# Kernel tuning notes

Hardware: AMD Instinct MI355X
Metric: run time of the kernel (lower is better)

The kernel has to match this reference:

```python
import jax, jax.numpy as jnp
import numpy as np

D_MODEL = 512
NUM_HEADS = 8
NUM_LAYERS = 4
SEQ_LEN = 2048
BATCH = 2
LN_EPS = 1e-5


def _layer_norm(x, g, b):
    mu = jnp.mean(x, axis=-1, keepdims=True)
    var = jnp.mean(jnp.square(x - mu), axis=-1, keepdims=True)
    return (x - mu) * jax.lax.rsqrt(var + LN_EPS) * g + b


def setup_inputs() -> dict:
    key = jax.random.key(0)
    ks = jax.random.split(key, 12)
    d, nl = D_MODEL, NUM_LAYERS
    s = 0.02
    return {
        "x": jax.random.normal(ks[0], (BATCH, SEQ_LEN, d), dtype=jnp.float32),
        "mask": jnp.zeros((1, 1, SEQ_LEN, SEQ_LEN), dtype=jnp.float32),
        "Wqkv": jax.random.normal(ks[1], (nl, d, 3 * d), dtype=jnp.float32) * s,
        "Wout": jax.random.normal(ks[2], (nl, d, d), dtype=jnp.float32) * s,
        "ln_g": jnp.ones((nl, d), dtype=jnp.float32),
        "ln_b": jnp.zeros((nl, d), dtype=jnp.float32),
        "W1": jax.random.normal(ks[3], (nl, d, 4 * d), dtype=jnp.float32) * s,
        "b1": jnp.zeros((nl, 4 * d), dtype=jnp.float32),
        "alpha": jnp.full((nl,), 0.01, dtype=jnp.float32),  # PReLU(init=0.01), scalar per block
        "W2": jax.random.normal(ks[4], (nl, 4 * d, d), dtype=jnp.float32) * s,
        "b2": jnp.zeros((nl, d), dtype=jnp.float32),
        "lnf_g": jnp.ones((d,), dtype=jnp.float32),
        "lnf_b": jnp.zeros((d,), dtype=jnp.float32),
    }


def _encoder(x, mask, Wqkv, Wout, ln_g, ln_b, W1, b1, alpha, W2, b2, lnf_g, lnf_b):
    B, L, d = x.shape
    H = NUM_HEADS
    dh = d // H
    scale = 1.0 / (d ** 0.5)  # NOTE: scales by sqrt(d_model), not head dim (as in source)

    def block(x, p):
        wqkv, wout, g, b, w1, b1_, a, w2, b2_ = p
        qkv = x @ wqkv  # [B, L, 3d]
        q, k, v = jnp.split(qkv, 3, axis=-1)
        # b l (h j) -> b h l j
        to_heads = lambda t: t.reshape(B, L, H, dh).transpose(0, 2, 1, 3)
        q, k, v = to_heads(q) * scale, to_heads(k), to_heads(v)
        e = jnp.einsum('bhlj,bhkj->bhlk', q, k) + mask  # [B, H, L, L]
        att = jnp.nan_to_num(jax.nn.softmax(e, axis=-1))
        # Faithful to source: repeated index takes the DIAGONAL of att,
        # then multiplies elementwise into v (NOT a matmul).
        out = jnp.einsum('bhll,bhlj->bhlj', att, v)
        out = out.transpose(0, 2, 1, 3).reshape(B, L, d)  # b h l j -> b l (h j)
        out = out @ wout
        out_att = _layer_norm(out + x, g, b)
        h = out_att @ w1 + b1_
        h = jnp.where(h >= 0, h, a * h)  # PReLU (dropout=0 in eval)
        h = h @ w2 + b2_
        # same LayerNorm params reused (same nn.LayerNorm instance in source)
        return _layer_norm(h + out_att, g, b), None

    params = (Wqkv, Wout, ln_g, ln_b, W1, b1, alpha, W2, b2)
    x, _ = jax.lax.scan(block, x, params)
    return _layer_norm(x, lnf_g, lnf_b)


def reference(x, mask, Wqkv, Wout, ln_g, ln_b, W1, b1, alpha, W2, b2, lnf_g, lnf_b):
    return _encoder(x, mask, Wqkv, Wout, ln_g, ln_b, W1, b1, alpha, W2, b2, lnf_g, lnf_b)
```

## Files before the change

### kernel.cpp

```cpp
#include <hip/hip_runtime.h>
#include <math.h>

typedef unsigned short u16;
typedef __attribute__((ext_vector_type(8))) short short8;
typedef __attribute__((ext_vector_type(4))) float f32x4;

#define SEQ 2048
#define NHEADS 8
#define NLAYERS 4
#define NROWS 4096
#define SCALE_QK_LOG2E 0.06376571201f
#define PART_STRIDE ((size_t)NROWS * 512)

#define GLOAD_LDS(gp, lp) __builtin_amdgcn_global_load_lds( \
    (const __attribute__((address_space(1))) uint4*)(gp), \
    (__attribute__((address_space(3))) uint4*)(lp), 16, 0, 0)

__device__ __forceinline__ float b2f(u16 u){
    union { unsigned int i; float f; } c; c.i = ((unsigned int)u) << 16; return c.f;
}
__device__ __forceinline__ u16 f2b(float f){
    union { float f; unsigned int i; } c; c.f = f;
    unsigned int x = c.i;
    unsigned int r = x + 0x7fffu + ((x >> 16) & 1u);
    return (u16)(r >> 16);
}
__device__ __forceinline__ void unpack8(uint4 u, float* f){
    f[0]=b2f(u.x & 0xffffu); f[1]=b2f(u.x >> 16);
    f[2]=b2f(u.y & 0xffffu); f[3]=b2f(u.y >> 16);
    f[4]=b2f(u.z & 0xffffu); f[5]=b2f(u.z >> 16);
    f[6]=b2f(u.w & 0xffffu); f[7]=b2f(u.w >> 16);
}
__device__ __forceinline__ uint4 pack8(const float* f){
    uint4 u;
    u.x = (unsigned)f2b(f[0]) | ((unsigned)f2b(f[1]) << 16);
    u.y = (unsigned)f2b(f[2]) | ((unsigned)f2b(f[3]) << 16);
    u.z = (unsigned)f2b(f[4]) | ((unsigned)f2b(f[5]) << 16);
    u.w = (unsigned)f2b(f[6]) | ((unsigned)f2b(f[7]) << 16);
    return u;
}

__global__ __launch_bounds__(256)
void cvt_f32_bf16(const float* __restrict__ in, u16* __restrict__ out, int n8){
    int i = blockIdx.x * 256 + threadIdx.x;
    if (i >= n8) return;
    const float4* p = (const float4*)(in + (size_t)i * 8);
    float4 a = p[0], b = p[1];
    float f[8] = {a.x, a.y, a.z, a.w, b.x, b.y, b.z, b.w};
    *((uint4*)(out + (size_t)i * 8)) = pack8(f);
}

__global__ __launch_bounds__(256)
void transpose_layer(const float* __restrict__ wqkv, const float* __restrict__ wout,
                     const float* __restrict__ w1,  const float* __restrict__ w2,
                     u16* __restrict__ qkvT, u16* __restrict__ woutT,
                     u16* __restrict__ w1T,  u16* __restrict__ w2T)
{
    __shared__ float tile[32][33];
    int tid = blockIdx.x;
    const float* src; u16* dst; int R, C, local;
    if (tid < 768)       { src = wqkv; dst = qkvT; R = 512;  C = 1536; local = tid; }
    else if (tid < 1024) { src = wout; dst = woutT; R = 512; C = 512;  local = tid - 768; }
    else if (tid < 2048) { src = w1;   dst = w1T;  R = 512;  C = 2048; local = tid - 1024; }
    else                 { src = w2;   dst = w2T;  R = 2048; C = 512;  local = tid - 2048; }
    int ctiles = C >> 5;
    int c0 = (local % ctiles) * 32, r0 = (local / ctiles) * 32;
    int tx = threadIdx.x & 31, ty = threadIdx.x >> 5;
#pragma unroll
    for (int i = 0; i < 4; i++){
        int r = r0 + ty + i * 8;
        tile[ty + i * 8][tx] = src[(size_t)r * C + c0 + tx];
    }
    __syncthreads();
#pragma unroll
    for (int i = 0; i < 4; i++){
        int c = c0 + ty + i * 8;
        dst[(size_t)c * R + r0 + tx] = f2b(tile[tx][ty + i * 8]);
    }
}

template<int BM, int BN, int SPLITS>
__global__ __launch_bounds__(256)
void gemm3(const u16* __restrict__ A, const u16* __restrict__ Bt,
           u16* __restrict__ C,
           const float* __restrict__ bias, const float* __restrict__ alphap,
           int N, int K)
{
    constexpr int NBY = NROWS / BM;
    constexpr int WAVES_M = BM / 64;
    constexpr int WAVES_N = 4 / WAVES_M;
    constexpr int WN = BN / WAVES_N;
    constexpr int MT = 4, NT = WN / 16;
    __shared__ __align__(16) u16 As[BM * 64];
    __shared__ __align__(16) u16 Bs[BN * 64];

    const int t = threadIdx.x;
    const int wave = t >> 6, lane = t & 63;
    const int quad = lane >> 4, l16 = lane & 15;
    const int wm = (WAVES_M == 2) ? (wave >> 1) : 0;
    const int wn = (WAVES_M == 2) ? (wave & 1) : wave;
    const int id = blockIdx.x;
    const int m0 = (id % NBY) * BM;
    const int n0 = (id / NBY) * BN;
    const int lr = lane >> 3;
    const int lc = (lane & 7) << 3;
    const int Ks = K / SPLITS;
    const int kbeg = blockIdx.z * Ks;

    f32x4 acc[MT][NT];
#pragma unroll
    for (int i = 0; i < MT; i++)
#pragma unroll
        for (int j = 0; j < NT; j++) acc[i][j] = (f32x4){0.f, 0.f, 0.f, 0.f};

    for (int kt = kbeg; kt < kbeg + Ks; kt += 64){
        __syncthreads();
#pragma unroll
        for (int j = 0; j < BM / 32; j++){
            int r0 = wave * 8 + j * 32;
            GLOAD_LDS(A + (size_t)(m0 + r0 + lr) * K + kt + lc, As + r0 * 64);
        }
#pragma unroll
        for (int j = 0; j < BN / 32; j++){
            int r0 = wave * 8 + j * 32;
            GLOAD_LDS(Bt + (size_t)(n0 + r0 + lr) * K + kt + lc, Bs + r0 * 64);
        }
        __syncthreads();
#pragma unroll
        for (int ks = 0; ks < 2; ks++){
            short8 af[MT], bf[NT];
#pragma unroll
            for (int mt = 0; mt < MT; mt++)
                af[mt] = *((const short8*)&As[(wm * 64 + mt * 16 + l16) * 64 + ks * 32 + quad * 8]);
#pragma unroll
            for (int nt = 0; nt < NT; nt++)
                bf[nt] = *((const short8*)&Bs[(wn * WN + nt * 16 + l16) * 64 + ks * 32 + quad * 8]);
#pragma unroll
            for (int mt = 0; mt < MT; mt++)
#pragma unroll
                for (int nt = 0; nt < NT; nt++)
                    acc[mt][nt] = __builtin_amdgcn_mfma_f32_16x16x32_bf16(af[mt], bf[nt], acc[mt][nt], 0, 0, 0);
        }
    }

    u16* Cp = (SPLITS > 1) ? (C + (size_t)blockIdx.z * PART_STRIDE) : C;
    const float aval = alphap ? alphap[0] : 0.f;
#pragma unroll
    for (int nt = 0; nt < NT; nt++){
        int col = n0 + wn * WN + nt * 16 + l16;
        float bv = (SPLITS == 1 && bias) ? bias[col] : 0.f;
#pragma unroll
        for (int mt = 0; mt < MT; mt++){
#pragma unroll
            for (int r = 0; r < 4; r++){
                int row = m0 + wm * 64 + mt * 16 + quad * 4 + r;
                float v = acc[mt][nt][r] + bv;
                if (SPLITS == 1 && alphap) v = (v >= 0.f) ? v : aval * v;
                Cp[(size_t)row * N + col] = f2b(v);
            }
        }
    }
}

__global__ __launch_bounds__(256)
void attn_scores2(const u16* __restrict__ qkv, float* __restrict__ rowsum_parts)
{
    __shared__ __align__(16) u16 Qs[128 * 64];
    __shared__ __align__(16) u16 Ks[128 * 64];
    const int t = threadIdx.x, wave = t >> 6, lane = t & 63;
    const int quad = lane >> 4, l16 = lane & 15;
    const int wm = wave >> 1, wn = wave & 1;
    const int id = blockIdx.x;
    const int bh = id & 15, ly = (id >> 4) & 15, ksp = id >> 8;
    const int b = bh >> 3, h = bh & 7;
    const int lr = lane >> 3, lc = (lane & 7) << 3;
    const size_t qbase = (size_t)(b * SEQ + ly * 128) * 1536 + h * 64;

#pragma unroll
    for (int j = 0; j < 4; j++){
        int r0 = wave * 8 + j * 32;
        GLOAD_LDS(qkv + qbase + (size_t)(r0 + lr) * 1536 + lc, Qs + r0 * 64);
    }

    float rs[4][4];
#pragma unroll
    for (int i = 0; i < 4; i++)
#pragma unroll
        for (int j = 0; j < 4; j++) rs[i][j] = 0.f;

    for (int kxi = 0; kxi < 4; kxi++){
        const int kx = ksp * 4 + kxi;
        const size_t kbase = (size_t)(b * SEQ + kx * 128) * 1536 + 512 + h * 64;
        __syncthreads();
#pragma unroll
        for (int j = 0; j < 4; j++){
            int r0 = wave * 8 + j * 32;
            GLOAD_LDS(qkv + kbase + (size_t)(r0 + lr) * 1536 + lc, Ks + r0 * 64);
        }
        __syncthreads();

        f32x4 acc[4][4];
#pragma unroll
        for (int i = 0; i < 4; i++)
#pragma unroll
            for (int j = 0; j < 4; j++) acc[i][j] = (f32x4){0.f, 0.f, 0.f, 0.f};
#pragma unroll
        for (int ks = 0; ks < 2; ks++){
            short8 af[4], bf[4];
#pragma unroll
            for (int mt = 0; mt < 4; mt++)
                af[mt] = *((const short8*)&Qs[(wm * 64 + mt * 16 + l16) * 64 + ks * 32 + quad * 8]);
#pragma unroll
            for (int nt = 0; nt < 4; nt++)
                bf[nt] = *((const short8*)&Ks[(wn * 64 + nt * 16 + l16) * 64 + ks * 32 + quad * 8]);
#pragma unroll
            for (int mt = 0; mt < 4; mt++)
#pragma unroll
                for (int nt = 0; nt < 4; nt++)
                    acc[mt][nt] = __builtin_amdgcn_mfma_f32_16x16x32_bf16(af[mt], bf[nt], acc[mt][nt], 0, 0, 0);
        }
#pragma unroll
        for (int mt = 0; mt < 4; mt++)
#pragma unroll
            for (int nt = 0; nt < 4; nt++)
#pragma unroll
                for (int r = 0; r < 4; r++)
                    rs[mt][r] += exp2f(acc[mt][nt][r] * SCALE_QK_LOG2E);
    }

#pragma unroll
    for (int off = 1; off < 16; off <<= 1){
#pragma unroll
        for (int mt = 0; mt < 4; mt++)
#pragma unroll
            for (int r = 0; r < 4; r++)
                rs[mt][r] += __shfl_xor(rs[mt][r], off, 64);
    }
    if (l16 == 0){
        const int part = ksp * 2 + wn;
        float* dst = rowsum_parts + (size_t)part * 16 * SEQ + (size_t)bh * SEQ + ly * 128;
#pragma unroll
        for (int mt = 0; mt < 4; mt++)
#pragma unroll
            for (int r = 0; r < 4; r++)
                dst[wm * 64 + mt * 16 + quad * 4 + r] = rs[mt][r];
    }
}

__global__ __launch_bounds__(256)
void attn_scale(const u16* __restrict__ qkv, const float* __restrict__ rowsum_parts,
                u16* __restrict__ attnb)
{
    int gid = blockIdx.x * 256 + threadIdx.x;
    int row = gid >> 6;
    int col = (gid & 63) << 3;
    int head = col >> 6;
    int b = row >> 11, l = row & 2047;
    size_t base = (size_t)row * 1536 + col;

    float qv[8], kv[8];
    unpack8(*((const uint4*)(qkv + base)), qv);
    unpack8(*((const uint4*)(qkv + base + 512)), kv);
    float dot = 0.f;
#pragma unroll
    for (int j = 0; j < 8; j++) dot += qv[j] * kv[j];
#pragma unroll
    for (int off = 1; off < 8; off <<= 1) dot += __shfl_xor(dot, off, 64);

    size_t idx = (size_t)(b * 8 + head) * SEQ + l;
    float rsum = 0.f;
#pragma unroll
    for (int p = 0; p < 8; p++) rsum += rowsum_parts[(size_t)p * 16 * SEQ + idx];
    float a = exp2f(dot * SCALE_QK_LOG2E) / rsum;

    float f[8];
    unpack8(*((const uint4*)(qkv + base + 1024)), f);
#pragma unroll
    for (int j = 0; j < 8; j++) f[j] *= a;
    *((uint4*)(attnb + (size_t)row * 512 + col)) = pack8(f);
}

__global__ __launch_bounds__(256)
void ln_kernel(const u16* __restrict__ res, int nparts,
               const float* __restrict__ bias, const u16* __restrict__ xin,
               const float* __restrict__ gg, const float* __restrict__ bb,
               u16* __restrict__ outb, float* __restrict__ outf)
{
    const int row = blockIdx.x * 4 + (threadIdx.x >> 6);
    const int lane = threadIdx.x & 63;
    const size_t base = (size_t)row * 512 + lane * 8;

    float v[8];
    unpack8(*((const uint4*)(xin + base)), v);
    for (int p = 0; p < nparts; p++){
        float rv[8];
        unpack8(*((const uint4*)(res + (size_t)p * PART_STRIDE + base)), rv);
#pragma unroll
        for (int j = 0; j < 8; j++) v[j] += rv[j];
    }
    if (bias){
        const float4* bp4 = (const float4*)(bias + lane * 8);
        float4 c0 = bp4[0], c1 = bp4[1];
        v[0] += c0.x; v[1] += c0.y; v[2] += c0.z; v[3] += c0.w;
        v[4] += c1.x; v[5] += c1.y; v[6] += c1.z; v[7] += c1.w;
    }
    float s = 0.f;
#pragma unroll
    for (int j = 0; j < 8; j++) s += v[j];
#pragma unroll
    for (int off = 32; off; off >>= 1) s += __shfl_xor(s, off, 64);
    float mu = s * (1.f / 512.f);
    float q = 0.f;
#pragma unroll
    for (int j = 0; j < 8; j++){ float d = v[j] - mu; q += d * d; }
#pragma unroll
    for (int off = 32; off; off >>= 1) q += __shfl_xor(q, off, 64);
    float rs = rsqrtf(q * (1.f / 512.f) + 1e-5f);

    const float4* gp = (const float4*)(gg + lane * 8);
    const float4* bp = (const float4*)(bb + lane * 8);
    float4 g0 = gp[0], g1 = gp[1], bb0 = bp[0], bb1 = bp[1];
    float gv[8] = {g0.x, g0.y, g0.z, g0.w, g1.x, g1.y, g1.z, g1.w};
    float bv[8] = {bb0.x, bb0.y, bb0.z, bb0.w, bb1.x, bb1.y, bb1.z, bb1.w};
    float o[8];
#pragma unroll
    for (int j = 0; j < 8; j++) o[j] = (v[j] - mu) * rs * gv[j] + bv[j];
    if (outb){
        *((uint4*)(outb + base)) = pack8(o);
    } else {
        float4* op = (float4*)(outf + base);
        op[0] = make_float4(o[0], o[1], o[2], o[3]);
        op[1] = make_float4(o[4], o[5], o[6], o[7]);
    }
}

extern "C" void kernel_launch(void* const* d_in, const int* in_sizes, int n_in,
                              void* d_out, int out_size, void* d_ws, size_t ws_size,
                              hipStream_t stream)
{
    const float* x_in  = (const float*)d_in[0];
    const float* Wqkv  = (const float*)d_in[2];
    const float* Wout  = (const float*)d_in[3];
    const float* ln_g  = (const float*)d_in[4];
    const float* ln_b  = (const float*)d_in[5];
    const float* W1    = (const float*)d_in[6];
    const float* b1    = (const float*)d_in[7];
    const float* alpha = (const float*)d_in[8];
    const float* W2    = (const float*)d_in[9];
    const float* b2    = (const float*)d_in[10];
    const float* lnf_g = (const float*)d_in[11];
    const float* lnf_b = (const float*)d_in[12];
    float* out = (float*)d_out;

    char* w = (char*)d_ws;
    u16* qkvT  = (u16*)w;  w += (size_t)1536 * 512 * 2;
    u16* woutT = (u16*)w;  w += (size_t)512 * 512 * 2;
    u16* w1T   = (u16*)w;  w += (size_t)2048 * 512 * 2;
    u16* w2T   = (u16*)w;  w += (size_t)512 * 2048 * 2;
    u16* big    = (u16*)w;  w += (size_t)NROWS * 2048 * 2;
    u16* x_cur  = (u16*)w;  w += (size_t)NROWS * 512 * 2;
    u16* attnb  = (u16*)w;  w += (size_t)NROWS * 512 * 2;
    u16* outatt = (u16*)w;  w += (size_t)NROWS * 512 * 2;
    u16* tmpb   = (u16*)w;  w += (size_t)4 * PART_STRIDE * 2;
    float* rowsum_parts = (float*)w; w += (size_t)8 * 2 * NHEADS * SEQ * 4;

    u16* qkvb = big;
    u16* hbuf = big;

    cvt_f32_bf16<<<NROWS * 512 / 8 / 256, 256, 0, stream>>>(x_in, x_cur, NROWS * 512 / 8);

    for (int l = 0; l < NLAYERS; l++){
        transpose_layer<<<3072, 256, 0, stream>>>(
            Wqkv + (size_t)l * 512 * 1536, Wout + (size_t)l * 512 * 512,
            W1 + (size_t)l * 512 * 2048,  W2 + (size_t)l * 2048 * 512,
            qkvT, woutT, w1T, w2T);

        gemm3<128, 64, 1><<<dim3(24 * 32), 256, 0, stream>>>(
            x_cur, qkvT, qkvb, nullptr, nullptr, 1536, 512);

        attn_scores2<<<1024, 256, 0, stream>>>(qkvb, rowsum_parts);
        attn_scale<<<NROWS * 512 / 8 / 256, 256, 0, stream>>>(qkvb, rowsum_parts, attnb);

        gemm3<64, 128, 2><<<dim3(4 * 64, 1, 2), 256, 0, stream>>>(
            attnb, woutT, tmpb, nullptr, nullptr, 512, 512);

        ln_kernel<<<NROWS / 4, 256, 0, stream>>>(tmpb, 2, nullptr, x_cur,
            ln_g + l * 512, ln_b + l * 512, outatt, nullptr);

        gemm3<128, 128, 1><<<dim3(16 * 32), 256, 0, stream>>>(
            outatt, w1T, hbuf, b1 + (size_t)l * 2048, alpha + l, 2048, 512);

        gemm3<64, 128, 4><<<dim3(4 * 64, 1, 4), 256, 0, stream>>>(
            hbuf, w2T, tmpb, nullptr, nullptr, 512, 2048);

        ln_kernel<<<NROWS / 4, 256, 0, stream>>>(tmpb, 4, b2 + (size_t)l * 512, outatt,
            ln_g + l * 512, ln_b + l * 512, x_cur, nullptr);
    }

    ln_kernel<<<NROWS / 4, 256, 0, stream>>>(nullptr, 0, nullptr, x_cur, lnf_g, lnf_b, nullptr, out);
}
```

Baseline: 537.5 us.

## Fuse attention row-sum and diagonal scaling; transpose all layer weights once

The two attention kernels (partial row sums written to global memory, then a separate scale pass) become one 512-thread kernel per (batch, head, 128-row block). It loops over all 16 key tiles, reduces row sums through shared memory, then scales V by the diagonal softmax weight in the same kernel. The per-layer weight transposes are replaced by a single launch covering all layers into a larger workspace. This cuts launches and global traffic, but attention now runs only 256 blocks with serialized key tiles instead of 1024 blocks, which lowers parallelism.

Result: slower. 574.4 us (+6.9%).

```diff
diff --git a/kernel.cpp b/kernel.cpp
--- a/kernel.cpp
+++ b/kernel.cpp
@@ -51,18 +51,19 @@
 }
 
 __global__ __launch_bounds__(256)
-void transpose_layer(const float* __restrict__ wqkv, const float* __restrict__ wout,
-                     const float* __restrict__ w1,  const float* __restrict__ w2,
-                     u16* __restrict__ qkvT, u16* __restrict__ woutT,
-                     u16* __restrict__ w1T,  u16* __restrict__ w2T)
+void transpose_all(const float* __restrict__ Wqkv, const float* __restrict__ Wout,
+                   const float* __restrict__ W1,  const float* __restrict__ W2,
+                   u16* __restrict__ qkvT, u16* __restrict__ woutT,
+                   u16* __restrict__ w1T,  u16* __restrict__ w2T)
 {
     __shared__ float tile[32][33];
-    int tid = blockIdx.x;
+    int l = blockIdx.x / 3072;
+    int tid = blockIdx.x % 3072;
     const float* src; u16* dst; int R, C, local;
-    if (tid < 768)       { src = wqkv; dst = qkvT; R = 512;  C = 1536; local = tid; }
-    else if (tid < 1024) { src = wout; dst = woutT; R = 512; C = 512;  local = tid - 768; }
-    else if (tid < 2048) { src = w1;   dst = w1T;  R = 512;  C = 2048; local = tid - 1024; }
-    else                 { src = w2;   dst = w2T;  R = 2048; C = 512;  local = tid - 2048; }
+    if (tid < 768)       { src = Wqkv + (size_t)l * 512 * 1536; dst = qkvT + (size_t)l * 1536 * 512; R = 512;  C = 1536; local = tid; }
+    else if (tid < 1024) { src = Wout + (size_t)l * 512 * 512;  dst = woutT + (size_t)l * 512 * 512; R = 512;  C = 512;  local = tid - 768; }
+    else if (tid < 2048) { src = W1 + (size_t)l * 512 * 2048;   dst = w1T + (size_t)l * 2048 * 512;  R = 512;  C = 2048; local = tid - 1024; }
+    else                 { src = W2 + (size_t)l * 2048 * 512;   dst = w2T + (size_t)l * 512 * 2048;  R = 2048; C = 512;  local = tid - 2048; }
     int ctiles = C >> 5;
     int c0 = (local % ctiles) * 32, r0 = (local / ctiles) * 32;
     int tx = threadIdx.x & 31, ty = threadIdx.x >> 5;
@@ -162,23 +163,26 @@
     }
 }
 
-__global__ __launch_bounds__(256)
-void attn_scores2(const u16* __restrict__ qkv, float* __restrict__ rowsum_parts)
+__global__ __launch_bounds__(512)
+void attn_fused(const u16* __restrict__ qkv, u16* __restrict__ attnb)
 {
     __shared__ __align__(16) u16 Qs[128 * 64];
     __shared__ __align__(16) u16 Ks[128 * 64];
+    __shared__ float psum[4][128];
+    __shared__ float rowsum[128];
+
     const int t = threadIdx.x, wave = t >> 6, lane = t & 63;
     const int quad = lane >> 4, l16 = lane & 15;
-    const int wm = wave >> 1, wn = wave & 1;
+    const int wm = wave >> 2, wn = wave & 3;
     const int id = blockIdx.x;
-    const int bh = id & 15, ly = (id >> 4) & 15, ksp = id >> 8;
+    const int ly = id & 15, bh = id >> 4;
     const int b = bh >> 3, h = bh & 7;
     const int lr = lane >> 3, lc = (lane & 7) << 3;
     const size_t qbase = (size_t)(b * SEQ + ly * 128) * 1536 + h * 64;
 
 #pragma unroll
-    for (int j = 0; j < 4; j++){
-        int r0 = wave * 8 + j * 32;
+    for (int j = 0; j < 2; j++){
+        int r0 = wave * 8 + j * 64;
         GLOAD_LDS(qkv + qbase + (size_t)(r0 + lr) * 1536 + lc, Qs + r0 * 64);
     }
 
@@ -188,41 +192,40 @@
 #pragma unroll
         for (int j = 0; j < 4; j++) rs[i][j] = 0.f;
 
-    for (int kxi = 0; kxi < 4; kxi++){
-        const int kx = ksp * 4 + kxi;
+    for (int kx = 0; kx < 16; kx++){
         const size_t kbase = (size_t)(b * SEQ + kx * 128) * 1536 + 512 + h * 64;
         __syncthreads();
 #pragma unroll
-        for (int j = 0; j < 4; j++){
-            int r0 = wave * 8 + j * 32;
+        for (int j = 0; j < 2; j++){
+            int r0 = wave * 8 + j * 64;
             GLOAD_LDS(qkv + kbase + (size_t)(r0 + lr) * 1536 + lc, Ks + r0 * 64);
         }
         __syncthreads();
 
-        f32x4 acc[4][4];
+        f32x4 acc[4][2];
 #pragma unroll
         for (int i = 0; i < 4; i++)
 #pragma unroll
-            for (int j = 0; j < 4; j++) acc[i][j] = (f32x4){0.f, 0.f, 0.f, 0.f};
+            for (int j = 0; j < 2; j++) acc[i][j] = (f32x4){0.f, 0.f, 0.f, 0.f};
 #pragma unroll
         for (int ks = 0; ks < 2; ks++){
-            short8 af[4], bf[4];
+            short8 af[4], bf[2];
 #pragma unroll
             for (int mt = 0; mt < 4; mt++)
                 af[mt] = *((const short8*)&Qs[(wm * 64 + mt * 16 + l16) * 64 + ks * 32 + quad * 8]);
 #pragma unroll
-            for (int nt = 0; nt < 4; nt++)
-                bf[nt] = *((const short8*)&Ks[(wn * 64 + nt * 16 + l16) * 64 + ks * 32 + quad * 8]);
+            for (int nt = 0; nt < 2; nt++)
+                bf[nt] = *((const short8*)&Ks[(wn * 32 + nt * 16 + l16) * 64 + ks * 32 + quad * 8]);
 #pragma unroll
             for (int mt = 0; mt < 4; mt++)
 #pragma unroll
-                for (int nt = 0; nt < 4; nt++)
+                for (int nt = 0; nt < 2; nt++)
                     acc[mt][nt] = __builtin_amdgcn_mfma_f32_16x16x32_bf16(af[mt], bf[nt], acc[mt][nt], 0, 0, 0);
         }
 #pragma unroll
         for (int mt = 0; mt < 4; mt++)
 #pragma unroll
-            for (int nt = 0; nt < 4; nt++)
+            for (int nt = 0; nt < 2; nt++)
 #pragma unroll
                 for (int r = 0; r < 4; r++)
                     rs[mt][r] += exp2f(acc[mt][nt][r] * SCALE_QK_LOG2E);
@@ -236,48 +239,38 @@
             for (int r = 0; r < 4; r++)
                 rs[mt][r] += __shfl_xor(rs[mt][r], off, 64);
     }
+    __syncthreads();
     if (l16 == 0){
-        const int part = ksp * 2 + wn;
-        float* dst = rowsum_parts + (size_t)part * 16 * SEQ + (size_t)bh * SEQ + ly * 128;
 #pragma unroll
         for (int mt = 0; mt < 4; mt++)
 #pragma unroll
             for (int r = 0; r < 4; r++)
-                dst[wm * 64 + mt * 16 + quad * 4 + r] = rs[mt][r];
-    }
-}
-
-__global__ __launch_bounds__(256)
-void attn_scale(const u16* __restrict__ qkv, const float* __restrict__ rowsum_parts,
-                u16* __restrict__ attnb)
-{
-    int gid = blockIdx.x * 256 + threadIdx.x;
-    int row = gid >> 6;
-    int col = (gid & 63) << 3;
-    int head = col >> 6;
-    int b = row >> 11, l = row & 2047;
-    size_t base = (size_t)row * 1536 + col;
-
-    float qv[8], kv[8];
-    unpack8(*((const uint4*)(qkv + base)), qv);
-    unpack8(*((const uint4*)(qkv + base + 512)), kv);
-    float dot = 0.f;
-#pragma unroll
-    for (int j = 0; j < 8; j++) dot += qv[j] * kv[j];
-#pragma unroll
-    for (int off = 1; off < 8; off <<= 1) dot += __shfl_xor(dot, off, 64);
-
-    size_t idx = (size_t)(b * 8 + head) * SEQ + l;
-    float rsum = 0.f;
-#pragma unroll
-    for (int p = 0; p < 8; p++) rsum += rowsum_parts[(size_t)p * 16 * SEQ + idx];
-    float a = exp2f(dot * SCALE_QK_LOG2E) / rsum;
-
-    float f[8];
-    unpack8(*((const uint4*)(qkv + base + 1024)), f);
-#pragma unroll
-    for (int j = 0; j < 8; j++) f[j] *= a;
-    *((uint4*)(attnb + (size_t)row * 512 + col)) = pack8(f);
+                psum[wn][wm * 64 + mt * 16 + quad * 4 + r] = rs[mt][r];
+    }
+    __syncthreads();
+    if (t < 128) rowsum[t] = psum[0][t] + psum[1][t] + psum[2][t] + psum[3][t];
+    __syncthreads();
+
+#pragma unroll 4
+    for (int i = 0; i < 16; i++){
+        int lrow = i * 8 + wave;
+        size_t rowg = (size_t)(b * SEQ + ly * 128 + lrow) * 1536;
+        int col = lane << 3;
+        float qv[8], kv[8];
+        unpack8(*((const uint4*)(qkv + rowg + col)), qv);
+        unpack8(*((const uint4*)(qkv + rowg + 512 + col)), kv);
+        float dot = 0.f;
+#pragma unroll
+        for (int j = 0; j < 8; j++) dot += qv[j] * kv[j];
+#pragma unroll
+        for (int off = 1; off < 8; off <<= 1) dot += __shfl_xor(dot, off, 64);
+        float a = exp2f(dot * SCALE_QK_LOG2E) / rowsum[lrow];
+        float f[8];
+        unpack8(*((const uint4*)(qkv + rowg + 1024 + col)), f);
+#pragma unroll
+        for (int j = 0; j < 8; j++) f[j] *= a;
+        *((uint4*)(attnb + (size_t)(b * SEQ + ly * 128 + lrow) * 512 + col)) = pack8(f);
+    }
 }
 
 __global__ __launch_bounds__(256)
@@ -353,45 +346,44 @@
     float* out = (float*)d_out;
 
     char* w = (char*)d_ws;
-    u16* qkvT  = (u16*)w;  w += (size_t)1536 * 512 * 2;
-    u16* woutT = (u16*)w;  w += (size_t)512 * 512 * 2;
-    u16* w1T   = (u16*)w;  w += (size_t)2048 * 512 * 2;
-    u16* w2T   = (u16*)w;  w += (size_t)512 * 2048 * 2;
+    u16* qkvT  = (u16*)w;  w += (size_t)NLAYERS * 1536 * 512 * 2;
+    u16* woutT = (u16*)w;  w += (size_t)NLAYERS * 512 * 512 * 2;
+    u16* w1T   = (u16*)w;  w += (size_t)NLAYERS * 2048 * 512 * 2;
+    u16* w2T   = (u16*)w;  w += (size_t)NLAYERS * 512 * 2048 * 2;
     u16* big    = (u16*)w;  w += (size_t)NROWS * 2048 * 2;
     u16* x_cur  = (u16*)w;  w += (size_t)NROWS * 512 * 2;
     u16* attnb  = (u16*)w;  w += (size_t)NROWS * 512 * 2;
     u16* outatt = (u16*)w;  w += (size_t)NROWS * 512 * 2;
     u16* tmpb   = (u16*)w;  w += (size_t)4 * PART_STRIDE * 2;
-    float* rowsum_parts = (float*)w; w += (size_t)8 * 2 * NHEADS * SEQ * 4;
 
     u16* qkvb = big;
     u16* hbuf = big;
 
     cvt_f32_bf16<<<NROWS * 512 / 8 / 256, 256, 0, stream>>>(x_in, x_cur, NROWS * 512 / 8);
+    transpose_all<<<NLAYERS * 3072, 256, 0, stream>>>(Wqkv, Wout, W1, W2, qkvT, woutT, w1T, w2T);
 
     for (int l = 0; l < NLAYERS; l++){
-        transpose_layer<<<3072, 256, 0, stream>>>(
-            Wqkv + (size_t)l * 512 * 1536, Wout + (size_t)l * 512 * 512,
-            W1 + (size_t)l * 512 * 2048,  W2 + (size_t)l * 2048 * 512,
-            qkvT, woutT, w1T, w2T);
+        const u16* wq  = qkvT  + (size_t)l * 1536 * 512;
+        const u16* wo  = woutT + (size_t)l * 512 * 512;
+        const u16* wf1 = w1T   + (size_t)l * 2048 * 512;
+        const u16* wf2 = w2T   + (size_t)l * 512 * 2048;
 
         gemm3<128, 64, 1><<<dim3(24 * 32), 256, 0, stream>>>(
-            x_cur, qkvT, qkvb, nullptr, nullptr, 1536, 512);
-
-        attn_scores2<<<1024, 256, 0, stream>>>(qkvb, rowsum_parts);
-        attn_scale<<<NROWS * 512 / 8 / 256, 256, 0, stream>>>(qkvb, rowsum_parts, attnb);
+            x_cur, wq, qkvb, nullptr, nullptr, 1536, 512);
+
+        attn_fused<<<256, 512, 0, stream>>>(qkvb, attnb);
 
         gemm3<64, 128, 2><<<dim3(4 * 64, 1, 2), 256, 0, stream>>>(
-            attnb, woutT, tmpb, nullptr, nullptr, 512, 512);
+            attnb, wo, tmpb, nullptr, nullptr, 512, 512);
 
         ln_kernel<<<NROWS / 4, 256, 0, stream>>>(tmpb, 2, nullptr, x_cur,
             ln_g + l * 512, ln_b + l * 512, outatt, nullptr);
 
         gemm3<128, 128, 1><<<dim3(16 * 32), 256, 0, stream>>>(
-            outatt, w1T, hbuf, b1 + (size_t)l * 2048, alpha + l, 2048, 512);
+            outatt, wf1, hbuf, b1 + (size_t)l * 2048, alpha + l, 2048, 512);
 
         gemm3<64, 128, 4><<<dim3(4 * 64, 1, 4), 256, 0, stream>>>(
-            hbuf, w2T, tmpb, nullptr, nullptr, 512, 2048);
+            hbuf, wf2, tmpb, nullptr, nullptr, 512, 2048);
 
         ln_kernel<<<NROWS / 4, 256, 0, stream>>>(tmpb, 4, b2 + (size_t)l * 512, outatt,
             ln_g + l * 512, ln_b + l * 512, x_cur, nullptr);
```
